# Optimization experiments

Measured on AMD Instinct MI355X. Metric: run time of the kernel, lower is better.

Reference implementation:

```python
import jax, jax.numpy as jnp
import numpy as np


def setup_inputs() -> dict:
    key = jax.random.key(0)
    ks = jax.random.split(key, 7)
    B, T, E, H = 4, 4096, 1024, 64
    return {
        "idx": jax.random.normal(ks[0], (B, T, E), dtype=jnp.float32),
        "Wq": jax.random.normal(ks[1], (E, H), dtype=jnp.float32) * (E ** -0.5),
        "bq": jax.random.normal(ks[2], (H,), dtype=jnp.float32) * 0.01,
        "Wk": jax.random.normal(ks[3], (E, H), dtype=jnp.float32) * (E ** -0.5),
        "bk": jax.random.normal(ks[4], (H,), dtype=jnp.float32) * 0.01,
        "Wv": jax.random.normal(ks[5], (E, H), dtype=jnp.float32) * (E ** -0.5),
        "bv": jax.random.normal(ks[6], (H,), dtype=jnp.float32) * 0.01,
    }


def reference(idx, Wq, bq, Wk, bk, Wv, bv):
    # idx: [B, T, E]
    d = idx.shape[-1]  # note: torch code scales by n_embd**-0.5, NOT head_size
    Q = idx @ Wq + bq  # [B, T, H]
    K = idx @ Wk + bk
    V = idx @ Wv + bv
    # scores; NOTE: original torch code calls wei.masked_fill(...) non-in-place
    # and discards the result, so no causal mask is applied. No softmax either.
    wei = jnp.einsum("bth,bsh->bts", Q, K) * (d ** -0.5)  # [B, T, T]
    out = jnp.einsum("bts,bsh->bth", wei, V)  # [B, T, H]
    return out
```

## Files before the change

### kernel.cpp

```cpp
#include <hip/hip_runtime.h>


typedef __attribute__((ext_vector_type(8))) short bf16x8;
typedef __attribute__((ext_vector_type(4))) float f32x4;

#define MFMA16(a, b, c) __builtin_amdgcn_mfma_f32_16x16x32_bf16((a), (b), (c), 0, 0, 0)

__device__ __forceinline__ unsigned short f2bf(float f) {
    unsigned int u = __float_as_uint(f);
    u += 0x7fffu + ((u >> 16) & 1u);
    return (unsigned short)(u >> 16);
}

__device__ __forceinline__ unsigned int cvtpk(float a, float b) {
    unsigned int r;
    asm("v_cvt_pk_bf16_f32 %0, %1, %2" : "=v"(r) : "v"(a), "v"(b));
    return r;
}

__device__ __forceinline__ bf16x8 cvt8(float4 lo, float4 hi) {
    union { unsigned int u[4]; bf16x8 v; } r;
    r.u[0] = cvtpk(lo.x, lo.y);
    r.u[1] = cvtpk(lo.z, lo.w);
    r.u[2] = cvtpk(hi.x, hi.y);
    r.u[3] = cvtpk(hi.z, hi.w);
    return r.v;
}

__global__ void prep(const float* __restrict__ Wq, const float* __restrict__ Wk,
                     const float* __restrict__ Wv, unsigned short* __restrict__ WB,
                     float* __restrict__ Mf8) {
    int t = blockIdx.x * 256 + threadIdx.x;
    for (int z = t; z < 131072; z += 24576) Mf8[z] = 0.f;
    int kki = t / 768;
    int rem = t - kki * 768;
    int nt = rem >> 6, lane = rem & 63;
    int n = nt * 16 + (lane & 15);
    int kb = kki * 32 + ((lane >> 4) * 8);
    int mm = n >> 6, h = n & 63;
    const float* W = (mm == 0) ? Wq : (mm == 1) ? Wk : Wv;
    float sc = (mm == 1) ? 0.03125f : 1.0f;
    bf16x8 v;
    #pragma unroll
    for (int j = 0; j < 8; j++) v[j] = (short)f2bf(W[(size_t)(kb + j) * 64 + h] * sc);
    *(bf16x8*)(WB + (size_t)t * 8) = v;
}

__global__ __launch_bounds__(256, 3) void qkv_m(
    const float* __restrict__ idx, const unsigned short* __restrict__ WB,
    const float* __restrict__ bq, const float* __restrict__ bk, const float* __restrict__ bv,
    unsigned short* __restrict__ Q, float* __restrict__ Mf8) {
    __shared__ unsigned short Lq[32 * 68];
    __shared__ unsigned short Lk[64 * 36];
    __shared__ unsigned short Lv[64 * 36];

    const int tid = threadIdx.x, lane = tid & 63, w = tid >> 6;
    const int r0 = blockIdx.x * 32;

    const float* A0 = idx + (size_t)(r0 + (lane & 15)) * 1024 + ((lane >> 4) * 8);
    const float* A1 = A0 + 16 * 1024;

    float4 aA0 = *(const float4*)(A0 + 0),  aA1 = *(const float4*)(A0 + 4);
    float4 aA2 = *(const float4*)(A1 + 0),  aA3 = *(const float4*)(A1 + 4);
    float4 aB0 = *(const float4*)(A0 + 32), aB1 = *(const float4*)(A0 + 36);
    float4 aB2 = *(const float4*)(A1 + 32), aB3 = *(const float4*)(A1 + 36);
    bf16x8 bE[3], bO[3];
    {
        const unsigned short* Bp0 = WB + (size_t)(lane * 8);
        const unsigned short* Bp1 = WB + (size_t)(12 * 64 + lane) * 8;
        #pragma unroll
        for (int j = 0; j < 3; j++) {
            bE[j] = *(const bf16x8*)(Bp0 + (w + j * 4) * 512);
            bO[j] = *(const bf16x8*)(Bp1 + (w + j * 4) * 512);
        }
    }

    const f32x4 z4 = {0.f, 0.f, 0.f, 0.f};
    f32x4 acc[2][3] = {{z4, z4, z4}, {z4, z4, z4}};

    for (int kk2 = 0; kk2 < 32; kk2 += 2) {
        {
            bf16x8 a0 = cvt8(aA0, aA1), a1 = cvt8(aA2, aA3);
            bf16x8 bu0 = bE[0], bu1 = bE[1], bu2 = bE[2];
            if (kk2 < 30) {
                const float* p0 = A0 + (kk2 + 2) * 32;
                const float* p1 = A1 + (kk2 + 2) * 32;
                aA0 = *(const float4*)p0; aA1 = *(const float4*)(p0 + 4);
                aA2 = *(const float4*)p1; aA3 = *(const float4*)(p1 + 4);
                const unsigned short* Bp = WB + (size_t)(((kk2 + 2) * 12) * 64 + lane) * 8;
                #pragma unroll
                for (int j = 0; j < 3; j++) bE[j] = *(const bf16x8*)(Bp + (w + j * 4) * 512);
            }
            acc[0][0] = MFMA16(a0, bu0, acc[0][0]);
            acc[1][0] = MFMA16(a1, bu0, acc[1][0]);
            acc[0][1] = MFMA16(a0, bu1, acc[0][1]);
            acc[1][1] = MFMA16(a1, bu1, acc[1][1]);
            acc[0][2] = MFMA16(a0, bu2, acc[0][2]);
            acc[1][2] = MFMA16(a1, bu2, acc[1][2]);
        }
        {
            bf16x8 a0 = cvt8(aB0, aB1), a1 = cvt8(aB2, aB3);
            bf16x8 bu0 = bO[0], bu1 = bO[1], bu2 = bO[2];
            if (kk2 < 30) {
                const float* p0 = A0 + (kk2 + 3) * 32;
                const float* p1 = A1 + (kk2 + 3) * 32;
                aB0 = *(const float4*)p0; aB1 = *(const float4*)(p0 + 4);
                aB2 = *(const float4*)p1; aB3 = *(const float4*)(p1 + 4);
                const unsigned short* Bp = WB + (size_t)(((kk2 + 3) * 12) * 64 + lane) * 8;
                #pragma unroll
                for (int j = 0; j < 3; j++) bO[j] = *(const bf16x8*)(Bp + (w + j * 4) * 512);
            }
            acc[0][0] = MFMA16(a0, bu0, acc[0][0]);
            acc[1][0] = MFMA16(a1, bu0, acc[1][0]);
            acc[0][1] = MFMA16(a0, bu1, acc[0][1]);
            acc[1][1] = MFMA16(a1, bu1, acc[1][1]);
            acc[0][2] = MFMA16(a0, bu2, acc[0][2]);
            acc[1][2] = MFMA16(a1, bu2, acc[1][2]);
        }
    }

    {
        const int h     = w * 16 + (lane & 15);
        const int rbase = (lane >> 4) * 4;
        float bias0 = bq[h], bias1 = bk[h] * 0.03125f, bias2 = bv[h];
        #pragma unroll
        for (int rf = 0; rf < 2; rf++) {
            #pragma unroll
            for (int reg = 0; reg < 4; reg++) {
                int r = rf * 16 + rbase + reg;
                Lq[r * 68 + h] = f2bf(acc[rf][0][reg] + bias0);
                Lk[h * 36 + r] = f2bf(acc[rf][1][reg] + bias1);
                Lv[h * 36 + r] = f2bf(acc[rf][2][reg] + bias2);
            }
        }
    }
    __syncthreads();

    {
        int qr = tid >> 3, qh = (tid & 7) * 8;
        *(uint4*)(Q + (size_t)(r0 + qr) * 64 + qh) = *(const uint4*)(Lq + qr * 68 + qh);
    }

    {
        const int tq = (lane >> 4) * 8;
        bf16x8 a = *(const bf16x8*)&Lk[(16 * w + (lane & 15)) * 36 + tq];
        const f32x4 z4b = {0.f, 0.f, 0.f, 0.f};
        f32x4 accM[4];
        #pragma unroll
        for (int nt = 0; nt < 4; nt++) {
            bf16x8 bb = *(const bf16x8*)&Lv[(nt * 16 + (lane & 15)) * 36 + tq];
            accM[nt] = MFMA16(a, bb, z4b);
        }
        float* P = Mf8 + (((size_t)(blockIdx.x & 7) * 4) + (size_t)(r0 >> 12)) * 4096;
        const int rowb = 16 * w + (lane >> 4) * 4;
        #pragma unroll
        for (int nt = 0; nt < 4; nt++)
            #pragma unroll
            for (int reg = 0; reg < 4; reg++)
                atomicAdd(&P[(rowb + reg) * 64 + nt * 16 + (lane & 15)], accM[nt][reg]);
    }
}

__global__ __launch_bounds__(256) void qm(
    const unsigned short* __restrict__ Q, const float* __restrict__ Mf8,
    float* __restrict__ out) {
    __shared__ unsigned short Lm[64 * 72];
    const int lane = threadIdx.x & 63, wave = threadIdx.x >> 6;
    const int r0 = blockIdx.x * 64;
    const int b  = r0 >> 12;
    {
        const int tt = threadIdx.x;
        int h1 = tt >> 2, h2c = (tt & 3) * 16;
        const float* Mp = Mf8 + (size_t)b * 4096 + h1 * 64 + h2c;
        float vals[16];
        #pragma unroll
        for (int u = 0; u < 16; u += 4) *(float4*)(vals + u) = *(const float4*)(Mp + u);
        #pragma unroll
        for (int c = 1; c < 8; c++) {
            const float* Mc = Mp + (size_t)c * 16384;
            #pragma unroll
            for (int u = 0; u < 16; u += 4) {
                float4 t = *(const float4*)(Mc + u);
                vals[u] += t.x; vals[u + 1] += t.y; vals[u + 2] += t.z; vals[u + 3] += t.w;
            }
        }
        #pragma unroll
        for (int u = 0; u < 16; u++) Lm[(h2c + u) * 72 + h1] = f2bf(vals[u]);
    }
    __syncthreads();
    const f32x4 z4 = {0.f, 0.f, 0.f, 0.f};
    f32x4 acc[4] = {z4, z4, z4, z4};
    const int rr = r0 + 16 * wave + (lane & 15);
    const int kq = (lane >> 4) * 8;
    #pragma unroll
    for (int ks = 0; ks < 2; ks++) {
        int k0 = ks * 32;
        bf16x8 a = *(const bf16x8*)&Q[(size_t)rr * 64 + k0 + kq];
        #pragma unroll
        for (int nt = 0; nt < 4; nt++) {
            bf16x8 bb = *(const bf16x8*)&Lm[(size_t)(nt * 16 + (lane & 15)) * 72 + k0 + kq];
            acc[nt] = MFMA16(a, bb, acc[nt]);
        }
    }
    const int rowb = r0 + 16 * wave + (lane >> 4) * 4;
    #pragma unroll
    for (int nt = 0; nt < 4; nt++)
        #pragma unroll
        for (int reg = 0; reg < 4; reg++)
            out[(size_t)(rowb + reg) * 64 + nt * 16 + (lane & 15)] = acc[nt][reg];
}

extern "C" void kernel_launch(void* const* d_in, const int* in_sizes, int n_in,
                              void* d_out, int out_size, void* d_ws, size_t ws_size,
                              hipStream_t stream) {
    const float* idx = (const float*)d_in[0];
    const float* Wq  = (const float*)d_in[1];
    const float* bq  = (const float*)d_in[2];
    const float* Wk  = (const float*)d_in[3];
    const float* bk  = (const float*)d_in[4];
    const float* Wv  = (const float*)d_in[5];
    const float* bv  = (const float*)d_in[6];
    float* out = (float*)d_out;

    char* ws = (char*)d_ws;
    unsigned short* WB  = (unsigned short*)(ws);
    float*          Mf8 = (float*)(ws + (1024u << 10));
    unsigned short* Q   = (unsigned short*)(ws + (2048u << 10));

    hipLaunchKernelGGL(prep,  dim3(96),  dim3(256), 0, stream, Wq, Wk, Wv, WB, Mf8);
    hipLaunchKernelGGL(qkv_m, dim3(512), dim3(256), 0, stream,
                       idx, WB, bq, bk, bv, Q, Mf8);
    hipLaunchKernelGGL(qm,    dim3(256), dim3(256), 0, stream, Q, Mf8, out);
}
```

Measured before the change: 138.5 us.

## Stage shared QKV weights in LDS via async global_load_lds with 1024-thread blocks

```diff
diff --git a/kernel.cpp b/kernel.cpp
--- a/kernel.cpp
+++ b/kernel.cpp
@@ -25,6 +25,12 @@
     r.u[2] = cvtpk(hi.x, hi.y);
     r.u[3] = cvtpk(hi.z, hi.w);
     return r.v;
+}
+
+__device__ __forceinline__ void gll16(const unsigned short* g, unsigned short* l) {
+    __builtin_amdgcn_global_load_lds(
+        (const __attribute__((address_space(1))) void*)g,
+        (__attribute__((address_space(3))) void*)l, 16, 0, 0);
 }
 
 __global__ void prep(const float* __restrict__ Wq, const float* __restrict__ Wk,
@@ -46,118 +52,113 @@
     *(bf16x8*)(WB + (size_t)t * 8) = v;
 }
 
-__global__ __launch_bounds__(256, 3) void qkv_m(
+__global__ __launch_bounds__(1024, 4) void qkv_m(
     const float* __restrict__ idx, const unsigned short* __restrict__ WB,
     const float* __restrict__ bq, const float* __restrict__ bk, const float* __restrict__ bv,
     unsigned short* __restrict__ Q, float* __restrict__ Mf8) {
-    __shared__ unsigned short Lq[32 * 68];
-    __shared__ unsigned short Lk[64 * 36];
-    __shared__ unsigned short Lv[64 * 36];
+    __shared__ unsigned short LDSB[4 * 6144];
 
     const int tid = threadIdx.x, lane = tid & 63, w = tid >> 6;
-    const int r0 = blockIdx.x * 32;
-
-    const float* A0 = idx + (size_t)(r0 + (lane & 15)) * 1024 + ((lane >> 4) * 8);
-    const float* A1 = A0 + 16 * 1024;
-
-    float4 aA0 = *(const float4*)(A0 + 0),  aA1 = *(const float4*)(A0 + 4);
-    float4 aA2 = *(const float4*)(A1 + 0),  aA3 = *(const float4*)(A1 + 4);
-    float4 aB0 = *(const float4*)(A0 + 32), aB1 = *(const float4*)(A0 + 36);
-    float4 aB2 = *(const float4*)(A1 + 32), aB3 = *(const float4*)(A1 + 36);
-    bf16x8 bE[3], bO[3];
-    {
-        const unsigned short* Bp0 = WB + (size_t)(lane * 8);
-        const unsigned short* Bp1 = WB + (size_t)(12 * 64 + lane) * 8;
-        #pragma unroll
-        for (int j = 0; j < 3; j++) {
-            bE[j] = *(const bf16x8*)(Bp0 + (w + j * 4) * 512);
-            bO[j] = *(const bf16x8*)(Bp1 + (w + j * 4) * 512);
-        }
-    }
+    const int wr = w >> 2, wc = w & 3;
+    const int r0 = blockIdx.x * 64;
+    const bool stager = (w < 12);
+
+    const float* A0 = idx + (size_t)(r0 + wr * 16 + (lane & 15)) * 1024 + ((lane >> 4) * 8);
+    const int soff = w * 512 + lane * 8;
+
+    if (stager) {
+        gll16(WB + 0 * 6144 + soff, LDSB + 0 * 6144 + soff);
+        gll16(WB + 1 * 6144 + soff, LDSB + 1 * 6144 + soff);
+    }
+    float4 aE0 = *(const float4*)(A0 + 0),  aE1 = *(const float4*)(A0 + 4);
+    float4 aO0 = *(const float4*)(A0 + 32), aO1 = *(const float4*)(A0 + 36);
 
     const f32x4 z4 = {0.f, 0.f, 0.f, 0.f};
-    f32x4 acc[2][3] = {{z4, z4, z4}, {z4, z4, z4}};
+    f32x4 acc[3] = {z4, z4, z4};
 
     for (int kk2 = 0; kk2 < 32; kk2 += 2) {
         {
-            bf16x8 a0 = cvt8(aA0, aA1), a1 = cvt8(aA2, aA3);
-            bf16x8 bu0 = bE[0], bu1 = bE[1], bu2 = bE[2];
+            const int k = kk2;
+            if (kk2 < 30) { asm volatile("s_waitcnt vmcnt(4)" ::: "memory"); }
+            else          { asm volatile("s_waitcnt vmcnt(2)" ::: "memory"); }
+            __builtin_amdgcn_s_barrier();
+            __builtin_amdgcn_sched_barrier(0);
+            const unsigned short* S = LDSB + (k & 3) * 6144;
+            bf16x8 b0 = *(const bf16x8*)(S + (wc + 0) * 512 + lane * 8);
+            bf16x8 b1 = *(const bf16x8*)(S + (wc + 4) * 512 + lane * 8);
+            bf16x8 b2 = *(const bf16x8*)(S + (wc + 8) * 512 + lane * 8);
+            float4 c0 = aE0, c1 = aE1;
             if (kk2 < 30) {
-                const float* p0 = A0 + (kk2 + 2) * 32;
-                const float* p1 = A1 + (kk2 + 2) * 32;
-                aA0 = *(const float4*)p0; aA1 = *(const float4*)(p0 + 4);
-                aA2 = *(const float4*)p1; aA3 = *(const float4*)(p1 + 4);
-                const unsigned short* Bp = WB + (size_t)(((kk2 + 2) * 12) * 64 + lane) * 8;
-                #pragma unroll
-                for (int j = 0; j < 3; j++) bE[j] = *(const bf16x8*)(Bp + (w + j * 4) * 512);
+                if (stager)
+                    gll16(WB + (k + 2) * 6144 + soff, LDSB + ((k + 2) & 3) * 6144 + soff);
+                const float* p = A0 + (k + 2) * 32;
+                aE0 = *(const float4*)p; aE1 = *(const float4*)(p + 4);
             }
-            acc[0][0] = MFMA16(a0, bu0, acc[0][0]);
-            acc[1][0] = MFMA16(a1, bu0, acc[1][0]);
-            acc[0][1] = MFMA16(a0, bu1, acc[0][1]);
-            acc[1][1] = MFMA16(a1, bu1, acc[1][1]);
-            acc[0][2] = MFMA16(a0, bu2, acc[0][2]);
-            acc[1][2] = MFMA16(a1, bu2, acc[1][2]);
+            bf16x8 a = cvt8(c0, c1);
+            acc[0] = MFMA16(a, b0, acc[0]);
+            acc[1] = MFMA16(a, b1, acc[1]);
+            acc[2] = MFMA16(a, b2, acc[2]);
         }
         {
-            bf16x8 a0 = cvt8(aB0, aB1), a1 = cvt8(aB2, aB3);
-            bf16x8 bu0 = bO[0], bu1 = bO[1], bu2 = bO[2];
+            const int k = kk2 + 1;
+            if (kk2 < 30) { asm volatile("s_waitcnt vmcnt(4)" ::: "memory"); }
+            else          { asm volatile("s_waitcnt vmcnt(2)" ::: "memory"); }
+            __builtin_amdgcn_s_barrier();
+            __builtin_amdgcn_sched_barrier(0);
+            const unsigned short* S = LDSB + (k & 3) * 6144;
+            bf16x8 b0 = *(const bf16x8*)(S + (wc + 0) * 512 + lane * 8);
+            bf16x8 b1 = *(const bf16x8*)(S + (wc + 4) * 512 + lane * 8);
+            bf16x8 b2 = *(const bf16x8*)(S + (wc + 8) * 512 + lane * 8);
+            float4 c0 = aO0, c1 = aO1;
             if (kk2 < 30) {
-                const float* p0 = A0 + (kk2 + 3) * 32;
-                const float* p1 = A1 + (kk2 + 3) * 32;
-                aB0 = *(const float4*)p0; aB1 = *(const float4*)(p0 + 4);
-                aB2 = *(const float4*)p1; aB3 = *(const float4*)(p1 + 4);
-                const unsigned short* Bp = WB + (size_t)(((kk2 + 3) * 12) * 64 + lane) * 8;
-                #pragma unroll
-                for (int j = 0; j < 3; j++) bO[j] = *(const bf16x8*)(Bp + (w + j * 4) * 512);
+                if (stager)
+                    gll16(WB + (k + 2) * 6144 + soff, LDSB + ((k + 2) & 3) * 6144 + soff);
+                const float* p = A0 + (k + 2) * 32;
+                aO0 = *(const float4*)p; aO1 = *(const float4*)(p + 4);
             }
-            acc[0][0] = MFMA16(a0, bu0, acc[0][0]);
-            acc[1][0] = MFMA16(a1, bu0, acc[1][0]);
-            acc[0][1] = MFMA16(a0, bu1, acc[0][1]);
-            acc[1][1] = MFMA16(a1, bu1, acc[1][1]);
-            acc[0][2] = MFMA16(a0, bu2, acc[0][2]);
-            acc[1][2] = MFMA16(a1, bu2, acc[1][2]);
-        }
-    }
-
-    {
-        const int h     = w * 16 + (lane & 15);
-        const int rbase = (lane >> 4) * 4;
-        float bias0 = bq[h], bias1 = bk[h] * 0.03125f, bias2 = bv[h];
-        #pragma unroll
-        for (int rf = 0; rf < 2; rf++) {
-            #pragma unroll
-            for (int reg = 0; reg < 4; reg++) {
-                int r = rf * 16 + rbase + reg;
-                Lq[r * 68 + h] = f2bf(acc[rf][0][reg] + bias0);
-                Lk[h * 36 + r] = f2bf(acc[rf][1][reg] + bias1);
-                Lv[h * 36 + r] = f2bf(acc[rf][2][reg] + bias2);
-            }
-        }
-    }
+            bf16x8 a = cvt8(c0, c1);
+            acc[0] = MFMA16(a, b0, acc[0]);
+            acc[1] = MFMA16(a, b1, acc[1]);
+            acc[2] = MFMA16(a, b2, acc[2]);
+        }
+    }
+
     __syncthreads();
-
-    {
-        int qr = tid >> 3, qh = (tid & 7) * 8;
-        *(uint4*)(Q + (size_t)(r0 + qr) * 64 + qh) = *(const uint4*)(Lq + qr * 68 + qh);
-    }
-
-    {
-        const int tq = (lane >> 4) * 8;
-        bf16x8 a = *(const bf16x8*)&Lk[(16 * w + (lane & 15)) * 36 + tq];
-        const f32x4 z4b = {0.f, 0.f, 0.f, 0.f};
-        f32x4 accM[4];
-        #pragma unroll
-        for (int nt = 0; nt < 4; nt++) {
-            bf16x8 bb = *(const bf16x8*)&Lv[(nt * 16 + (lane & 15)) * 36 + tq];
-            accM[nt] = MFMA16(a, bb, z4b);
-        }
-        float* P = Mf8 + (((size_t)(blockIdx.x & 7) * 4) + (size_t)(r0 >> 12)) * 4096;
-        const int rowb = 16 * w + (lane >> 4) * 4;
-        #pragma unroll
-        for (int nt = 0; nt < 4; nt++)
-            #pragma unroll
-            for (int reg = 0; reg < 4; reg++)
-                atomicAdd(&P[(rowb + reg) * 64 + nt * 16 + (lane & 15)], accM[nt][reg]);
+    unsigned short* Lq = LDSB;
+    unsigned short* Lk = LDSB + 4608;
+    unsigned short* Lv = LDSB + 9216;
+    {
+        const int col   = wc * 16 + (lane & 15);
+        const int rbase = wr * 16 + (lane >> 4) * 4;
+        float b0v = bq[col], b1v = bk[col] * 0.03125f, b2v = bv[col];
+        #pragma unroll
+        for (int reg = 0; reg < 4; reg++) {
+            int r = rbase + reg;
+            Lq[r * 72 + col] = f2bf(acc[0][reg] + b0v);
+            Lk[col * 72 + r] = f2bf(acc[1][reg] + b1v);
+            Lv[col * 72 + r] = f2bf(acc[2][reg] + b2v);
+        }
+    }
+    __syncthreads();
+
+    {
+        int row = tid >> 4, c4 = (tid & 15) * 4;
+        *(uint2*)(Q + (size_t)(r0 + row) * 64 + c4) = *(const uint2*)(Lq + row * 72 + c4);
+    }
+
+    {
+        f32x4 accM = z4;
+        #pragma unroll
+        for (int ts = 0; ts < 64; ts += 32) {
+            bf16x8 ka = *(const bf16x8*)(Lk + (wr * 16 + (lane & 15)) * 72 + ts + (lane >> 4) * 8);
+            bf16x8 vb = *(const bf16x8*)(Lv + (wc * 16 + (lane & 15)) * 72 + ts + (lane >> 4) * 8);
+            accM = MFMA16(ka, vb, accM);
+        }
+        float* P = Mf8 + ((size_t)(blockIdx.x & 7) * 4 + (size_t)(r0 >> 12)) * 4096;
+        const int rowb = wr * 16 + (lane >> 4) * 4;
+        #pragma unroll
+        for (int reg = 0; reg < 4; reg++)
+            atomicAdd(&P[(rowb + reg) * 64 + wc * 16 + (lane & 15)], accM[reg]);
     }
 }
 
@@ -227,8 +228,8 @@
     float*          Mf8 = (float*)(ws + (1024u << 10));
     unsigned short* Q   = (unsigned short*)(ws + (2048u << 10));
 
-    hipLaunchKernelGGL(prep,  dim3(96),  dim3(256), 0, stream, Wq, Wk, Wv, WB, Mf8);
-    hipLaunchKernelGGL(qkv_m, dim3(512), dim3(256), 0, stream,
+    hipLaunchKernelGGL(prep,  dim3(96),  dim3(256),  0, stream, Wq, Wk, Wv, WB, Mf8);
+    hipLaunchKernelGGL(qkv_m, dim3(256), dim3(1024), 0, stream,
                        idx, WB, bq, bk, bv, Q, Mf8);
-    hipLaunchKernelGGL(qm,    dim3(256), dim3(256), 0, stream, Q, Mf8, out);
-}
+    hipLaunchKernelGGL(qm,    dim3(256), dim3(256),  0, stream, Q, Mf8, out);
+}
```

Measured after the change: 144.7 us. 4.4% more time.
